# Kernel optimization log

Measured on AMD Instinct MI355X. Metric: run time of the kernel, lower is better.

The kernel has to match this reference:

```python
import jax, jax.numpy as jnp
import numpy as np

D_MODEL = 1024
NUM_HEADS = 16
DK = D_MODEL // NUM_HEADS


def setup_inputs() -> dict:
    key = jax.random.key(0)
    ks = jax.random.split(key, 12)
    B, S, D = 2, 2048, D_MODEL
    s = 1.0 / np.sqrt(D)
    inp = {
        "Q": jax.random.normal(ks[0], (B, S, D), jnp.float32),
        "K": jax.random.normal(ks[1], (B, S, D), jnp.float32),
        "V": jax.random.normal(ks[2], (B, S, D), jnp.float32),
        "Wq": jax.random.uniform(ks[3], (D, D), jnp.float32, -s, s),
        "bq": jax.random.uniform(ks[4], (D,), jnp.float32, -s, s),
        "Wk": jax.random.uniform(ks[5], (D, D), jnp.float32, -s, s),
        "bk": jax.random.uniform(ks[6], (D,), jnp.float32, -s, s),
        "Wv": jax.random.uniform(ks[7], (D, D), jnp.float32, -s, s),
        "bv": jax.random.uniform(ks[8], (D,), jnp.float32, -s, s),
        "Wo": jax.random.uniform(ks[9], (D, D), jnp.float32, -s, s),
        "bo": jax.random.uniform(ks[10], (D,), jnp.float32, -s, s),
    }
    return inp


def reference(Q, K, V, Wq, bq, Wk, bk, Wv, bv, Wo, bo):
    B, S, D = Q.shape
    H, dk = NUM_HEADS, DK
    # projections (torch Linear: x @ W.T + b), split heads -> [B,H,S,dk]
    q = (Q @ Wq.T + bq).reshape(B, S, H, dk).transpose(0, 2, 1, 3)
    k = (K @ Wk.T + bk).reshape(B, S, H, dk).transpose(0, 2, 1, 3)
    v = (V @ Wv.T + bv).reshape(B, S, H, dk).transpose(0, 2, 1, 3)
    scores = jnp.einsum("bhqd,bhkd->bhqk", q, k) / jnp.sqrt(jnp.asarray(dk, q.dtype))
    attn = jax.nn.softmax(scores, axis=-1)
    out = jnp.einsum("bhqk,bhkd->bhqd", attn, v)  # [B,H,S,dk]
    out = out.transpose(0, 2, 1, 3).reshape(B, S, D)
    return out @ Wo.T + bo
```

## Files before the change

### kernel.cpp

```cpp
#include <hip/hip_runtime.h>
#include <stdint.h>


#define AS1 __attribute__((address_space(1)))
#define AS3 __attribute__((address_space(3)))

typedef unsigned short u16;
typedef short s16x8 __attribute__((ext_vector_type(8)));
typedef float f32x4 __attribute__((ext_vector_type(4)));
typedef u16   u16x4 __attribute__((ext_vector_type(4)));

#if defined(__has_builtin)
#if __has_builtin(__builtin_amdgcn_exp2f)
#define EXP2F(x) __builtin_amdgcn_exp2f(x)
#else
#define EXP2F(x) exp2f(x)
#endif
#else
#define EXP2F(x) exp2f(x)
#endif

__device__ __forceinline__ u16 f2b(float f) {
  union { float f; uint32_t u; } v;
  v.f = f;
  uint32_t r = (v.u + 0x7fffu + ((v.u >> 16) & 1u)) >> 16;
  return (u16)r;
}

__device__ __forceinline__ uint32_t cvtpk(float lo, float hi) {
  uint32_t r;
  asm("v_cvt_pk_bf16_f32 %0, %1, %2" : "=v"(r) : "v"(lo), "v"(hi));
  return r;
}

__device__ __forceinline__ f32x4 mfma16(s16x8 a, s16x8 b, f32x4 c) {
  return __builtin_amdgcn_mfma_f32_16x16x32_bf16(a, b, c, 0, 0, 0);
}

__device__ __forceinline__ s16x8 ld_g16(const u16* p) {
  return *reinterpret_cast<const s16x8*>(p);
}

__device__ __forceinline__ void stage16(const u16* g, u16* lds_base) {
  __builtin_amdgcn_global_load_lds((const AS1 unsigned int*)g,
                                   (AS3 unsigned int*)lds_base, 16, 0, 0);
}

struct CvtArgs {
  const float* src[7];
  u16* dst[7];
  int cum[8];
};

__global__ __launch_bounds__(256) void cvt_all(CvtArgs a) {
  const int bx = blockIdx.x;
  int seg = 0;
#pragma unroll
  for (int i = 1; i < 7; ++i) seg += (bx >= a.cum[i]) ? 1 : 0;
  const int off = (bx - a.cum[seg]) * 256 + threadIdx.x;
  float4 f = reinterpret_cast<const float4*>(a.src[seg])[off];
  union { u16 u[4]; uint64_t q; } o;
  o.u[0] = f2b(f.x); o.u[1] = f2b(f.y); o.u[2] = f2b(f.z); o.u[3] = f2b(f.w);
  reinterpret_cast<uint64_t*>(a.dst[seg])[off] = o.q;
}

template <int MODE>
__global__ __launch_bounds__(256) void gemm_bt(const u16* __restrict__ Abase,
                                               const u16* __restrict__ Wbase,
                                               const float* __restrict__ bias0,
                                               const float* __restrict__ bias1,
                                               const float* __restrict__ bias2,
                                               u16* __restrict__ outb,
                                               u16* __restrict__ vtout,
                                               float* __restrict__ outf) {
  __shared__ u16 As[2][128 * 64];
  __shared__ u16 Bs[2][128 * 64];
  const int tid = threadIdx.x;
  const int lane = tid & 63;
  const int w = tid >> 6;
  const int wr = w >> 1, wc = w & 1;

  const int bid = blockIdx.y * 8 + blockIdx.x;
  const int sw = (bid & 7) * 32 + (bid >> 3);
  const int n0 = (sw & 7) * 128;
  const int m0 = (sw >> 3) * 128;
  const int z = (MODE == 0) ? blockIdx.z : 0;
  const float QSC = 0.18033688011112042f;

  const u16* A = Abase + (size_t)z * (4096u * 1024u);
  const u16* W = Wbase + (size_t)z * (1024u * 1024u);
  const float* bias = (MODE == 0) ? (z == 0 ? bias0 : (z == 1 ? bias1 : bias2)) : bias0;
  u16* ob = (MODE == 0) ? (outb + (size_t)z * (4096u * 1024u)) : nullptr;

  const int l15 = lane & 15, l4 = lane >> 4;

  const int sr = lane >> 3;
  const int sx = lane & 7;
  const u16* gA[4];
  const u16* gB[4];
#pragma unroll
  for (int j = 0; j < 4; ++j) {
    const int row = w * 32 + j * 8 + sr;
    const int lc = ((sx ^ (row & 7)) << 3);
    gA[j] = A + (size_t)(m0 + row) * 1024 + lc;
    gB[j] = W + (size_t)(n0 + row) * 1024 + lc;
  }

  f32x4 acc[4][4];
#pragma unroll
  for (int i = 0; i < 4; ++i)
#pragma unroll
    for (int j = 0; j < 4; ++j) acc[i][j] = {0.f, 0.f, 0.f, 0.f};

#pragma unroll
  for (int j = 0; j < 4; ++j) {
    stage16(gA[j], &As[0][(w * 32 + j * 8) * 64]);
    stage16(gB[j], &Bs[0][(w * 32 + j * 8) * 64]);
  }
  __syncthreads();

#pragma unroll 2
  for (int t = 0; t < 16; ++t) {
    const int cur = t & 1;
    if (t + 1 < 16) {
      const int kt = (t + 1) * 64;
#pragma unroll
      for (int j = 0; j < 4; ++j) {
        stage16(gA[j] + kt, &As[cur ^ 1][(w * 32 + j * 8) * 64]);
        stage16(gB[j] + kt, &Bs[cur ^ 1][(w * 32 + j * 8) * 64]);
      }
    }
#pragma unroll
    for (int ks = 0; ks < 2; ++ks) {
      s16x8 af[4], bf[4];
#pragma unroll
      for (int mi = 0; mi < 4; ++mi) {
        const int row = wr * 64 + mi * 16 + l15;
        const int sc_ = (((ks << 2) | l4) ^ (l15 & 7)) << 3;
        af[mi] = *(const s16x8*)&As[cur][row * 64 + sc_];
      }
#pragma unroll
      for (int ni = 0; ni < 4; ++ni) {
        const int row = wc * 64 + ni * 16 + l15;
        const int sc_ = (((ks << 2) | l4) ^ (l15 & 7)) << 3;
        bf[ni] = *(const s16x8*)&Bs[cur][row * 64 + sc_];
      }
      __builtin_amdgcn_s_setprio(1);
#pragma unroll
      for (int mi = 0; mi < 4; ++mi)
#pragma unroll
        for (int ni = 0; ni < 4; ++ni)
          acc[mi][ni] = mfma16(af[mi], bf[ni], acc[mi][ni]);
      __builtin_amdgcn_s_setprio(0);
    }
    __syncthreads();
  }

#pragma unroll
  for (int ni = 0; ni < 4; ++ni) {
    const int col = n0 + wc * 64 + ni * 16 + l15;
    const float bv = bias[col];
#pragma unroll
    for (int mi = 0; mi < 4; ++mi) {
      const int row0 = m0 + wr * 64 + mi * 16 + l4 * 4;
      if (MODE == 0 && z == 2) {
        const int b = row0 >> 11, s0 = row0 & 2047;
        const int pos0 = (s0 & ~31) | ((s0 & 12) << 1) | ((s0 & 16) >> 2);
        const int h = col >> 6, d = col & 63;
        u16x4 pk = {f2b(acc[mi][ni][0] + bv), f2b(acc[mi][ni][1] + bv),
                    f2b(acc[mi][ni][2] + bv), f2b(acc[mi][ni][3] + bv)};
        *(u16x4*)&vtout[((size_t)(b * 16 + h) * 64 + d) * 2048 + pos0] = pk;
      } else {
#pragma unroll
        for (int r = 0; r < 4; ++r) {
          float val = acc[mi][ni][r] + bv;
          const int row = row0 + r;
          if (MODE == 0) {
            if (z == 0) val *= QSC;
            const int b = row >> 11, s = row & 2047;
            const int h = col >> 6, d = col & 63;
            ob[((size_t)(b * 16 + h) * 2048 + s) * 64 + d] = f2b(val);
          } else {
            outf[(size_t)row * 1024 + col] = val;
          }
        }
      }
    }
  }
}

__global__ __launch_bounds__(512, 4) void fattn(const u16* __restrict__ qp,
                                                const u16* __restrict__ kp,
                                                const u16* __restrict__ vt,
                                                u16* __restrict__ ao) {
  __shared__ u16 Kt[2][4096];
  __shared__ u16 Vt[2][4096];

  const int lane = threadIdx.x & 63;
  const int w = threadIdx.x >> 6;
  const int bh = blockIdx.y;
  const int b = bh >> 4, h = bh & 15;
  const int q0 = blockIdx.x * 128 + w * 16;
  const u16* qb = qp + (size_t)bh * (2048 * 64);
  const u16* kb = kp + (size_t)bh * (2048 * 64);
  const u16* vb = vt + (size_t)bh * (64 * 2048);
  const int l15 = lane & 15, l4 = lane >> 4;
  const float THR = 8.0f;

  const int srow = (w << 3) + (lane >> 3);
  const int c0 = (((lane & 7) ^ (srow & 7)) << 3);

  s16x8 qa[2];
#pragma unroll
  for (int ks = 0; ks < 2; ++ks)
    qa[ks] = ld_g16(qb + (size_t)(q0 + l15) * 64 + ks * 32 + l4 * 8);

  s16x8 onesf = {(short)0x3F80, (short)0x3F80, (short)0x3F80, (short)0x3F80,
                 (short)0x3F80, (short)0x3F80, (short)0x3F80, (short)0x3F80};

  f32x4 o[4];
  f32x4 o5 = {0.f, 0.f, 0.f, 0.f};
  float mrun = -1e30f;
#pragma unroll
  for (int ni = 0; ni < 4; ++ni) o[ni] = {0.f, 0.f, 0.f, 0.f};

  stage16(kb + (size_t)srow * 64 + c0, &Kt[0][w * 512]);
  stage16(vb + (size_t)srow * 2048 + c0, &Vt[0][w * 512]);
  __syncthreads();

#pragma unroll 2
  for (int t = 0; t < 32; ++t) {
    const int cur = t & 1;
    if (t + 1 < 32) {
      const int kk = (t + 1) << 6;
      stage16(kb + (size_t)(kk + srow) * 64 + c0, &Kt[cur ^ 1][w * 512]);
      stage16(vb + (size_t)srow * 2048 + kk + c0, &Vt[cur ^ 1][w * 512]);
    }

    f32x4 sc[4];
#pragma unroll
    for (int nk = 0; nk < 4; ++nk) sc[nk] = {0.f, 0.f, 0.f, 0.f};
#pragma unroll
    for (int ks = 0; ks < 2; ++ks) {
      s16x8 kf[4];
#pragma unroll
      for (int nk = 0; nk < 4; ++nk) {
        const int row = nk * 16 + l15;
        const int scx = (((ks << 2) | l4) ^ (l15 & 7)) << 3;
        kf[nk] = *(const s16x8*)&Kt[cur][row * 64 + scx];
      }
      __builtin_amdgcn_s_setprio(1);
#pragma unroll
      for (int nk = 0; nk < 4; ++nk)
        sc[nk] = mfma16(kf[nk], qa[ks], sc[nk]);
      __builtin_amdgcn_s_setprio(0);
    }

    float m01 = fmaxf(fmaxf(sc[0][0], sc[0][1]), fmaxf(sc[0][2], sc[0][3]));
    float m23 = fmaxf(fmaxf(sc[1][0], sc[1][1]), fmaxf(sc[1][2], sc[1][3]));
    float m45 = fmaxf(fmaxf(sc[2][0], sc[2][1]), fmaxf(sc[2][2], sc[2][3]));
    float m67 = fmaxf(fmaxf(sc[3][0], sc[3][1]), fmaxf(sc[3][2], sc[3][3]));
    float m = fmaxf(fmaxf(m01, m23), fmaxf(m45, m67));
    m = fmaxf(m, __shfl_xor(m, 16));
    m = fmaxf(m, __shfl_xor(m, 32));
    const float smax = m;

    if (__any(smax > mrun + THR)) {
      float mn = fmaxf(mrun, smax);
      float alpha = EXP2F(mrun - mn);
      mrun = mn;
#pragma unroll
      for (int r = 0; r < 4; ++r) {
        float ar = __shfl(alpha, l4 * 4 + r);
#pragma unroll
        for (int ni = 0; ni < 4; ++ni) o[ni][r] *= ar;
        o5[r] *= ar;
      }
    }

    float p[4][4];
#pragma unroll
    for (int nk = 0; nk < 4; ++nk)
#pragma unroll
      for (int r = 0; r < 4; ++r)
        p[nk][r] = EXP2F(sc[nk][r] - mrun);

#pragma unroll
    for (int ks = 0; ks < 2; ++ks) {
      union { uint32_t d[4]; s16x8 v; } pa;
      pa.d[0] = cvtpk(p[2 * ks][0], p[2 * ks][1]);
      pa.d[1] = cvtpk(p[2 * ks][2], p[2 * ks][3]);
      pa.d[2] = cvtpk(p[2 * ks + 1][0], p[2 * ks + 1][1]);
      pa.d[3] = cvtpk(p[2 * ks + 1][2], p[2 * ks + 1][3]);
      s16x8 vf[4];
#pragma unroll
      for (int ni = 0; ni < 4; ++ni) {
        const int row = ni * 16 + l15;
        const int scv = (((ks << 2) | l4) ^ (l15 & 7)) << 3;
        vf[ni] = *(const s16x8*)&Vt[cur][row * 64 + scv];
      }
      __builtin_amdgcn_s_setprio(1);
#pragma unroll
      for (int ni = 0; ni < 4; ++ni)
        o[ni] = mfma16(pa.v, vf[ni], o[ni]);
      o5 = mfma16(pa.v, onesf, o5);
      __builtin_amdgcn_s_setprio(0);
    }

    __syncthreads();
  }

#pragma unroll
  for (int r = 0; r < 4; ++r) {
    float inv = 1.0f / o5[r];
    int row = b * 2048 + q0 + l4 * 4 + r;
#pragma unroll
    for (int ni = 0; ni < 4; ++ni)
      ao[(size_t)row * 1024 + h * 64 + ni * 16 + l15] = f2b(o[ni][r] * inv);
  }
}

extern "C" void kernel_launch(void* const* d_in, const int* in_sizes, int n_in,
                              void* d_out, int out_size, void* d_ws, size_t ws_size,
                              hipStream_t stream) {
  const float* Q  = (const float*)d_in[0];
  const float* K  = (const float*)d_in[1];
  const float* V  = (const float*)d_in[2];
  const float* Wq = (const float*)d_in[3];
  const float* bq = (const float*)d_in[4];
  const float* Wk = (const float*)d_in[5];
  const float* bk = (const float*)d_in[6];
  const float* Wv = (const float*)d_in[7];
  const float* bv = (const float*)d_in[8];
  const float* Wo = (const float*)d_in[9];
  const float* bo = (const float*)d_in[10];
  float* out = (float*)d_out;

  const size_t NI = (size_t)4096 * 1024;
  const size_t NW = (size_t)1024 * 1024;
  u16* XB  = (u16*)d_ws;
  u16* WB  = XB + 3 * NI;
  u16* QKV = WB + 4 * NW;
  u16* VT  = QKV + 3 * NI;
  u16* AO  = VT + NI;

  CvtArgs ca;
  ca.src[0] = Q;  ca.dst[0] = XB;
  ca.src[1] = K;  ca.dst[1] = XB + NI;
  ca.src[2] = V;  ca.dst[2] = XB + 2 * NI;
  ca.src[3] = Wq; ca.dst[3] = WB;
  ca.src[4] = Wk; ca.dst[4] = WB + NW;
  ca.src[5] = Wv; ca.dst[5] = WB + 2 * NW;
  ca.src[6] = Wo; ca.dst[6] = WB + 3 * NW;
  ca.cum[0] = 0;     ca.cum[1] = 4096;  ca.cum[2] = 8192;  ca.cum[3] = 12288;
  ca.cum[4] = 13312; ca.cum[5] = 14336; ca.cum[6] = 15360; ca.cum[7] = 16384;
  cvt_all<<<dim3(16384), 256, 0, stream>>>(ca);

  gemm_bt<0><<<dim3(8, 32, 3), 256, 0, stream>>>(XB, WB, bq, bk, bv, QKV, VT, nullptr);
  fattn<<<dim3(16, 32), 512, 0, stream>>>(QKV, QKV + NI, VT, AO);
  gemm_bt<1><<<dim3(8, 32, 1), 256, 0, stream>>>(AO, WB + 3 * NW, bo, nullptr, nullptr,
                                                 nullptr, nullptr, out);
}
```

Baseline: 129.1 us.

## Process two query tiles per wave in flash attention to reuse K/V fragments

Each wave now handles 32 query rows (two 16-row tiles) instead of 16, so every K and V fragment read from LDS feeds twice as many MFMAs, and the grid is halved. The running max is folded into the score accumulator's initial value so the exponent needs no subtraction, and the row max uses v_max3. The cost is higher register pressure (launch bounds relaxed from 4 to 2 blocks per CU) and only 256 blocks, which may leave CUs underfilled on a large GPU.

```diff
diff --git a/kernel.cpp b/kernel.cpp
--- a/kernel.cpp
+++ b/kernel.cpp
@@ -30,6 +30,12 @@
 __device__ __forceinline__ uint32_t cvtpk(float lo, float hi) {
   uint32_t r;
   asm("v_cvt_pk_bf16_f32 %0, %1, %2" : "=v"(r) : "v"(lo), "v"(hi));
+  return r;
+}
+
+__device__ __forceinline__ float max3f(float a, float b, float c) {
+  float r;
+  asm("v_max3_f32 %0, %1, %2, %3" : "=v"(r) : "v"(a), "v"(b), "v"(c));
   return r;
 }
 
@@ -189,7 +195,7 @@
   }
 }
 
-__global__ __launch_bounds__(512, 4) void fattn(const u16* __restrict__ qp,
+__global__ __launch_bounds__(512, 2) void fattn(const u16* __restrict__ qp,
                                                 const u16* __restrict__ kp,
                                                 const u16* __restrict__ vt,
                                                 u16* __restrict__ ao) {
@@ -200,7 +206,7 @@
   const int w = threadIdx.x >> 6;
   const int bh = blockIdx.y;
   const int b = bh >> 4, h = bh & 15;
-  const int q0 = blockIdx.x * 128 + w * 16;
+  const int q0 = blockIdx.x * 256 + w * 32;
   const u16* qb = qp + (size_t)bh * (2048 * 64);
   const u16* kb = kp + (size_t)bh * (2048 * 64);
   const u16* vb = vt + (size_t)bh * (64 * 2048);
@@ -210,19 +216,23 @@
   const int srow = (w << 3) + (lane >> 3);
   const int c0 = (((lane & 7) ^ (srow & 7)) << 3);
 
-  s16x8 qa[2];
-#pragma unroll
-  for (int ks = 0; ks < 2; ++ks)
-    qa[ks] = ld_g16(qb + (size_t)(q0 + l15) * 64 + ks * 32 + l4 * 8);
+  s16x8 qa[2][2];
+#pragma unroll
+  for (int mi = 0; mi < 2; ++mi)
+#pragma unroll
+    for (int ks = 0; ks < 2; ++ks)
+      qa[mi][ks] = ld_g16(qb + (size_t)(q0 + mi * 16 + l15) * 64 + ks * 32 + l4 * 8);
 
   s16x8 onesf = {(short)0x3F80, (short)0x3F80, (short)0x3F80, (short)0x3F80,
                  (short)0x3F80, (short)0x3F80, (short)0x3F80, (short)0x3F80};
 
-  f32x4 o[4];
-  f32x4 o5 = {0.f, 0.f, 0.f, 0.f};
-  float mrun = -1e30f;
-#pragma unroll
-  for (int ni = 0; ni < 4; ++ni) o[ni] = {0.f, 0.f, 0.f, 0.f};
+  f32x4 o[2][4];
+  f32x4 o5[2] = {{0.f, 0.f, 0.f, 0.f}, {0.f, 0.f, 0.f, 0.f}};
+  float mrun[2] = {0.f, 0.f};
+#pragma unroll
+  for (int mi = 0; mi < 2; ++mi)
+#pragma unroll
+    for (int ni = 0; ni < 4; ++ni) o[mi][ni] = {0.f, 0.f, 0.f, 0.f};
 
   stage16(kb + (size_t)srow * 64 + c0, &Kt[0][w * 512]);
   stage16(vb + (size_t)srow * 2048 + c0, &Vt[0][w * 512]);
@@ -237,9 +247,13 @@
       stage16(vb + (size_t)srow * 2048 + kk + c0, &Vt[cur ^ 1][w * 512]);
     }
 
-    f32x4 sc[4];
-#pragma unroll
-    for (int nk = 0; nk < 4; ++nk) sc[nk] = {0.f, 0.f, 0.f, 0.f};
+    f32x4 sc[2][4];
+#pragma unroll
+    for (int mi = 0; mi < 2; ++mi) {
+      const float ini = -mrun[mi];
+#pragma unroll
+      for (int nk = 0; nk < 4; ++nk) sc[mi][nk] = {ini, ini, ini, ini};
+    }
 #pragma unroll
     for (int ks = 0; ks < 2; ++ks) {
       s16x8 kf[4];
@@ -251,73 +265,91 @@
       }
       __builtin_amdgcn_s_setprio(1);
 #pragma unroll
+      for (int mi = 0; mi < 2; ++mi)
+#pragma unroll
+        for (int nk = 0; nk < 4; ++nk)
+          sc[mi][nk] = mfma16(kf[nk], qa[mi][ks], sc[mi][nk]);
+      __builtin_amdgcn_s_setprio(0);
+    }
+
+    float mrel[2];
+#pragma unroll
+    for (int mi = 0; mi < 2; ++mi) {
+      float a = max3f(sc[mi][0][0], sc[mi][0][1], sc[mi][0][2]);
+      float c = max3f(sc[mi][1][0], sc[mi][1][1], sc[mi][1][2]);
+      float d = max3f(sc[mi][2][0], sc[mi][2][1], sc[mi][2][2]);
+      float e = max3f(sc[mi][3][0], sc[mi][3][1], sc[mi][3][2]);
+      float f0 = max3f(sc[mi][0][3], sc[mi][1][3], sc[mi][2][3]);
+      float m = max3f(max3f(a, c, d), max3f(e, f0, sc[mi][3][3]), -1e30f);
+      m = fmaxf(m, __shfl_xor(m, 16));
+      m = fmaxf(m, __shfl_xor(m, 32));
+      mrel[mi] = m;
+    }
+
+    if (__any((mrel[0] > THR) | (mrel[1] > THR))) {
+#pragma unroll
+      for (int mi = 0; mi < 2; ++mi) {
+        const float d = fmaxf(mrel[mi], 0.f);
+        mrun[mi] += d;
+        const float alpha = EXP2F(-d);
+#pragma unroll
+        for (int r = 0; r < 4; ++r) {
+          float ar = __shfl(alpha, l4 * 4 + r);
+#pragma unroll
+          for (int ni = 0; ni < 4; ++ni) o[mi][ni][r] *= ar;
+          o5[mi][r] *= ar;
+        }
+#pragma unroll
+        for (int nk = 0; nk < 4; ++nk)
+#pragma unroll
+          for (int r = 0; r < 4; ++r) sc[mi][nk][r] -= d;
+      }
+    }
+
+#pragma unroll
+    for (int mi = 0; mi < 2; ++mi) {
+      float p[4][4];
+#pragma unroll
       for (int nk = 0; nk < 4; ++nk)
-        sc[nk] = mfma16(kf[nk], qa[ks], sc[nk]);
-      __builtin_amdgcn_s_setprio(0);
-    }
-
-    float m01 = fmaxf(fmaxf(sc[0][0], sc[0][1]), fmaxf(sc[0][2], sc[0][3]));
-    float m23 = fmaxf(fmaxf(sc[1][0], sc[1][1]), fmaxf(sc[1][2], sc[1][3]));
-    float m45 = fmaxf(fmaxf(sc[2][0], sc[2][1]), fmaxf(sc[2][2], sc[2][3]));
-    float m67 = fmaxf(fmaxf(sc[3][0], sc[3][1]), fmaxf(sc[3][2], sc[3][3]));
-    float m = fmaxf(fmaxf(m01, m23), fmaxf(m45, m67));
-    m = fmaxf(m, __shfl_xor(m, 16));
-    m = fmaxf(m, __shfl_xor(m, 32));
-    const float smax = m;
-
-    if (__any(smax > mrun + THR)) {
-      float mn = fmaxf(mrun, smax);
-      float alpha = EXP2F(mrun - mn);
-      mrun = mn;
-#pragma unroll
-      for (int r = 0; r < 4; ++r) {
-        float ar = __shfl(alpha, l4 * 4 + r);
-#pragma unroll
-        for (int ni = 0; ni < 4; ++ni) o[ni][r] *= ar;
-        o5[r] *= ar;
-      }
-    }
-
-    float p[4][4];
-#pragma unroll
-    for (int nk = 0; nk < 4; ++nk)
-#pragma unroll
-      for (int r = 0; r < 4; ++r)
-        p[nk][r] = EXP2F(sc[nk][r] - mrun);
-
-#pragma unroll
-    for (int ks = 0; ks < 2; ++ks) {
-      union { uint32_t d[4]; s16x8 v; } pa;
-      pa.d[0] = cvtpk(p[2 * ks][0], p[2 * ks][1]);
-      pa.d[1] = cvtpk(p[2 * ks][2], p[2 * ks][3]);
-      pa.d[2] = cvtpk(p[2 * ks + 1][0], p[2 * ks + 1][1]);
-      pa.d[3] = cvtpk(p[2 * ks + 1][2], p[2 * ks + 1][3]);
-      s16x8 vf[4];
-#pragma unroll
-      for (int ni = 0; ni < 4; ++ni) {
-        const int row = ni * 16 + l15;
-        const int scv = (((ks << 2) | l4) ^ (l15 & 7)) << 3;
-        vf[ni] = *(const s16x8*)&Vt[cur][row * 64 + scv];
-      }
-      __builtin_amdgcn_s_setprio(1);
+#pragma unroll
+        for (int r = 0; r < 4; ++r)
+          p[nk][r] = EXP2F(sc[mi][nk][r]);
+#pragma unroll
+      for (int ks = 0; ks < 2; ++ks) {
+        union { uint32_t d[4]; s16x8 v; } pa;
+        pa.d[0] = cvtpk(p[2 * ks][0], p[2 * ks][1]);
+        pa.d[1] = cvtpk(p[2 * ks][2], p[2 * ks][3]);
+        pa.d[2] = cvtpk(p[2 * ks + 1][0], p[2 * ks + 1][1]);
+        pa.d[3] = cvtpk(p[2 * ks + 1][2], p[2 * ks + 1][3]);
+        s16x8 vf[4];
+#pragma unroll
+        for (int ni = 0; ni < 4; ++ni) {
+          const int row = ni * 16 + l15;
+          const int scv = (((ks << 2) | l4) ^ (l15 & 7)) << 3;
+          vf[ni] = *(const s16x8*)&Vt[cur][row * 64 + scv];
+        }
+        __builtin_amdgcn_s_setprio(1);
+#pragma unroll
+        for (int ni = 0; ni < 4; ++ni)
+          o[mi][ni] = mfma16(pa.v, vf[ni], o[mi][ni]);
+        o5[mi] = mfma16(pa.v, onesf, o5[mi]);
+        __builtin_amdgcn_s_setprio(0);
+      }
+    }
+
+    __syncthreads();
+  }
+
+#pragma unroll
+  for (int mi = 0; mi < 2; ++mi)
+#pragma unroll
+    for (int r = 0; r < 4; ++r) {
+      float inv = 1.0f / o5[mi][r];
+      int row = b * 2048 + q0 + mi * 16 + l4 * 4 + r;
 #pragma unroll
       for (int ni = 0; ni < 4; ++ni)
-        o[ni] = mfma16(pa.v, vf[ni], o[ni]);
-      o5 = mfma16(pa.v, onesf, o5);
-      __builtin_amdgcn_s_setprio(0);
-    }
-
-    __syncthreads();
-  }
-
-#pragma unroll
-  for (int r = 0; r < 4; ++r) {
-    float inv = 1.0f / o5[r];
-    int row = b * 2048 + q0 + l4 * 4 + r;
-#pragma unroll
-    for (int ni = 0; ni < 4; ++ni)
-      ao[(size_t)row * 1024 + h * 64 + ni * 16 + l15] = f2b(o[ni][r] * inv);
-  }
+        ao[(size_t)row * 1024 + h * 64 + ni * 16 + l15] = f2b(o[mi][ni][r] * inv);
+    }
 }
 
 extern "C" void kernel_launch(void* const* d_in, const int* in_sizes, int n_in,
@@ -357,7 +389,7 @@
   cvt_all<<<dim3(16384), 256, 0, stream>>>(ca);
 
   gemm_bt<0><<<dim3(8, 32, 3), 256, 0, stream>>>(XB, WB, bq, bk, bv, QKV, VT, nullptr);
-  fattn<<<dim3(16, 32), 512, 0, stream>>>(QKV, QKV + NI, VT, AO);
+  fattn<<<dim3(8, 32), 512, 0, stream>>>(QKV, QKV + NI, VT, AO);
   gemm_bt<1><<<dim3(8, 32, 1), 256, 0, stream>>>(AO, WB + 3 * NW, bo, nullptr, nullptr,
                                                  nullptr, nullptr, out);
 }
```

Result: no change. 127.3 us (-1.4%).

## Switch flash attention to 32x32x16 MFMA with 32 query rows per wave

Applied to the files above, without the earlier changes.

Rewrites the attention inner loop to use 32x32x16 bf16 MFMAs, with each wave owning 32 query rows. The grid is halved and launch bounds are relaxed to match. The running max is folded into the score accumulator's initial value, and the row sum is accumulated with VALU adds instead of an extra MFMA against a ones vector. V^T's permuted layout in the projection GEMM is changed to match the new MFMA operand order. This cuts MFMA instruction count and LDS fragment reloads per tile, at the cost of higher register pressure, lower occupancy and fewer blocks (256) in flight.

```diff
diff --git a/kernel.cpp b/kernel.cpp
--- a/kernel.cpp
+++ b/kernel.cpp
@@ -8,6 +8,7 @@
 typedef unsigned short u16;
 typedef short s16x8 __attribute__((ext_vector_type(8)));
 typedef float f32x4 __attribute__((ext_vector_type(4)));
+typedef float f32x16 __attribute__((ext_vector_type(16)));
 typedef u16   u16x4 __attribute__((ext_vector_type(4)));
 
 #if defined(__has_builtin)
@@ -33,8 +34,18 @@
   return r;
 }
 
+__device__ __forceinline__ float max3f(float a, float b, float c) {
+  float r;
+  asm("v_max3_f32 %0, %1, %2, %3" : "=v"(r) : "v"(a), "v"(b), "v"(c));
+  return r;
+}
+
 __device__ __forceinline__ f32x4 mfma16(s16x8 a, s16x8 b, f32x4 c) {
   return __builtin_amdgcn_mfma_f32_16x16x32_bf16(a, b, c, 0, 0, 0);
+}
+
+__device__ __forceinline__ f32x16 mfma32(s16x8 a, s16x8 b, f32x16 c) {
+  return __builtin_amdgcn_mfma_f32_32x32x16_bf16(a, b, c, 0, 0, 0);
 }
 
 __device__ __forceinline__ s16x8 ld_g16(const u16* p) {
@@ -165,7 +176,7 @@
       const int row0 = m0 + wr * 64 + mi * 16 + l4 * 4;
       if (MODE == 0 && z == 2) {
         const int b = row0 >> 11, s0 = row0 & 2047;
-        const int pos0 = (s0 & ~31) | ((s0 & 12) << 1) | ((s0 & 16) >> 2);
+        const int pos0 = (s0 & ~15) | ((s0 & 4) << 1) | ((s0 & 8) >> 1);
         const int h = col >> 6, d = col & 63;
         u16x4 pk = {f2b(acc[mi][ni][0] + bv), f2b(acc[mi][ni][1] + bv),
                     f2b(acc[mi][ni][2] + bv), f2b(acc[mi][ni][3] + bv)};
@@ -189,7 +200,7 @@
   }
 }
 
-__global__ __launch_bounds__(512, 4) void fattn(const u16* __restrict__ qp,
+__global__ __launch_bounds__(512, 2) void fattn(const u16* __restrict__ qp,
                                                 const u16* __restrict__ kp,
                                                 const u16* __restrict__ vt,
                                                 u16* __restrict__ ao) {
@@ -200,29 +211,27 @@
   const int w = threadIdx.x >> 6;
   const int bh = blockIdx.y;
   const int b = bh >> 4, h = bh & 15;
-  const int q0 = blockIdx.x * 128 + w * 16;
+  const int q0 = blockIdx.x * 256 + w * 32;
   const u16* qb = qp + (size_t)bh * (2048 * 64);
   const u16* kb = kp + (size_t)bh * (2048 * 64);
   const u16* vb = vt + (size_t)bh * (64 * 2048);
-  const int l15 = lane & 15, l4 = lane >> 4;
+  const int l31 = lane & 31, hl = lane >> 5;
+  const int x7 = l31 & 7;
   const float THR = 8.0f;
 
   const int srow = (w << 3) + (lane >> 3);
   const int c0 = (((lane & 7) ^ (srow & 7)) << 3);
 
-  s16x8 qa[2];
-#pragma unroll
-  for (int ks = 0; ks < 2; ++ks)
-    qa[ks] = ld_g16(qb + (size_t)(q0 + l15) * 64 + ks * 32 + l4 * 8);
-
-  s16x8 onesf = {(short)0x3F80, (short)0x3F80, (short)0x3F80, (short)0x3F80,
-                 (short)0x3F80, (short)0x3F80, (short)0x3F80, (short)0x3F80};
-
-  f32x4 o[4];
-  f32x4 o5 = {0.f, 0.f, 0.f, 0.f};
-  float mrun = -1e30f;
-#pragma unroll
-  for (int ni = 0; ni < 4; ++ni) o[ni] = {0.f, 0.f, 0.f, 0.f};
+  s16x8 qa[4];
+#pragma unroll
+  for (int kc = 0; kc < 4; ++kc)
+    qa[kc] = ld_g16(qb + (size_t)(q0 + l31) * 64 + kc * 16 + hl * 8);
+
+  f32x16 o[2];
+  float lsum = 0.f;
+  float mrun = 0.f;
+#pragma unroll
+  for (int r = 0; r < 16; ++r) { o[0][r] = 0.f; o[1][r] = 0.f; }
 
   stage16(kb + (size_t)srow * 64 + c0, &Kt[0][w * 512]);
   stage16(vb + (size_t)srow * 2048 + c0, &Vt[0][w * 512]);
@@ -237,86 +246,83 @@
       stage16(vb + (size_t)srow * 2048 + kk + c0, &Vt[cur ^ 1][w * 512]);
     }
 
-    f32x4 sc[4];
-#pragma unroll
-    for (int nk = 0; nk < 4; ++nk) sc[nk] = {0.f, 0.f, 0.f, 0.f};
-#pragma unroll
-    for (int ks = 0; ks < 2; ++ks) {
+    f32x16 sc[2];
+#pragma unroll
+    for (int r = 0; r < 16; ++r) { sc[0][r] = -mrun; sc[1][r] = -mrun; }
+#pragma unroll
+    for (int nk = 0; nk < 2; ++nk) {
       s16x8 kf[4];
 #pragma unroll
-      for (int nk = 0; nk < 4; ++nk) {
-        const int row = nk * 16 + l15;
-        const int scx = (((ks << 2) | l4) ^ (l15 & 7)) << 3;
-        kf[nk] = *(const s16x8*)&Kt[cur][row * 64 + scx];
-      }
+      for (int kc = 0; kc < 4; ++kc)
+        kf[kc] = *(const s16x8*)&Kt[cur][(nk * 32 + l31) * 64 +
+                                         ((((kc << 1) | hl) ^ x7) << 3)];
       __builtin_amdgcn_s_setprio(1);
 #pragma unroll
-      for (int nk = 0; nk < 4; ++nk)
-        sc[nk] = mfma16(kf[nk], qa[ks], sc[nk]);
+      for (int kc = 0; kc < 4; ++kc)
+        sc[nk] = mfma32(kf[kc], qa[kc], sc[nk]);
       __builtin_amdgcn_s_setprio(0);
     }
 
-    float m01 = fmaxf(fmaxf(sc[0][0], sc[0][1]), fmaxf(sc[0][2], sc[0][3]));
-    float m23 = fmaxf(fmaxf(sc[1][0], sc[1][1]), fmaxf(sc[1][2], sc[1][3]));
-    float m45 = fmaxf(fmaxf(sc[2][0], sc[2][1]), fmaxf(sc[2][2], sc[2][3]));
-    float m67 = fmaxf(fmaxf(sc[3][0], sc[3][1]), fmaxf(sc[3][2], sc[3][3]));
-    float m = fmaxf(fmaxf(m01, m23), fmaxf(m45, m67));
-    m = fmaxf(m, __shfl_xor(m, 16));
+    float m = -1e30f;
+#pragma unroll
+    for (int nk = 0; nk < 2; ++nk)
+#pragma unroll
+      for (int r = 0; r < 16; r += 2)
+        m = max3f(m, sc[nk][r], sc[nk][r + 1]);
     m = fmaxf(m, __shfl_xor(m, 32));
-    const float smax = m;
-
-    if (__any(smax > mrun + THR)) {
-      float mn = fmaxf(mrun, smax);
-      float alpha = EXP2F(mrun - mn);
-      mrun = mn;
-#pragma unroll
-      for (int r = 0; r < 4; ++r) {
-        float ar = __shfl(alpha, l4 * 4 + r);
-#pragma unroll
-        for (int ni = 0; ni < 4; ++ni) o[ni][r] *= ar;
-        o5[r] *= ar;
-      }
-    }
-
-    float p[4][4];
-#pragma unroll
-    for (int nk = 0; nk < 4; ++nk)
-#pragma unroll
-      for (int r = 0; r < 4; ++r)
-        p[nk][r] = EXP2F(sc[nk][r] - mrun);
-
-#pragma unroll
-    for (int ks = 0; ks < 2; ++ks) {
-      union { uint32_t d[4]; s16x8 v; } pa;
-      pa.d[0] = cvtpk(p[2 * ks][0], p[2 * ks][1]);
-      pa.d[1] = cvtpk(p[2 * ks][2], p[2 * ks][3]);
-      pa.d[2] = cvtpk(p[2 * ks + 1][0], p[2 * ks + 1][1]);
-      pa.d[3] = cvtpk(p[2 * ks + 1][2], p[2 * ks + 1][3]);
-      s16x8 vf[4];
-#pragma unroll
-      for (int ni = 0; ni < 4; ++ni) {
-        const int row = ni * 16 + l15;
-        const int scv = (((ks << 2) | l4) ^ (l15 & 7)) << 3;
-        vf[ni] = *(const s16x8*)&Vt[cur][row * 64 + scv];
-      }
-      __builtin_amdgcn_s_setprio(1);
-#pragma unroll
-      for (int ni = 0; ni < 4; ++ni)
-        o[ni] = mfma16(pa.v, vf[ni], o[ni]);
-      o5 = mfma16(pa.v, onesf, o5);
-      __builtin_amdgcn_s_setprio(0);
+
+    if (__any(m > THR)) {
+      const float d = fmaxf(m, 0.f);
+      mrun += d;
+      const float alpha = EXP2F(-d);
+      lsum *= alpha;
+#pragma unroll
+      for (int r = 0; r < 16; ++r) { sc[0][r] -= d; sc[1][r] -= d; }
+#pragma unroll
+      for (int r = 0; r < 16; ++r) {
+        float ar = __shfl(alpha, (r & 3) + 8 * (r >> 2) + 4 * hl);
+        o[0][r] *= ar; o[1][r] *= ar;
+      }
+    }
+
+#pragma unroll
+    for (int nk = 0; nk < 2; ++nk) {
+      float p[16];
+#pragma unroll
+      for (int r = 0; r < 16; ++r) p[r] = EXP2F(sc[nk][r]);
+#pragma unroll
+      for (int r = 0; r < 16; ++r) lsum += p[r];
+#pragma unroll
+      for (int kc = 0; kc < 2; ++kc) {
+        union { uint32_t d[4]; s16x8 v; } pa;
+        pa.d[0] = cvtpk(p[kc * 8 + 0], p[kc * 8 + 1]);
+        pa.d[1] = cvtpk(p[kc * 8 + 2], p[kc * 8 + 3]);
+        pa.d[2] = cvtpk(p[kc * 8 + 4], p[kc * 8 + 5]);
+        pa.d[3] = cvtpk(p[kc * 8 + 6], p[kc * 8 + 7]);
+        const int chunk = nk * 4 + kc * 2 + hl;
+#pragma unroll
+        for (int dt = 0; dt < 2; ++dt) {
+          s16x8 vf = *(const s16x8*)&Vt[cur][(dt * 32 + l31) * 64 +
+                                             ((chunk ^ x7) << 3)];
+          __builtin_amdgcn_s_setprio(1);
+          o[dt] = mfma32(pa.v, vf, o[dt]);
+          __builtin_amdgcn_s_setprio(0);
+        }
+      }
     }
 
     __syncthreads();
   }
 
-#pragma unroll
-  for (int r = 0; r < 4; ++r) {
-    float inv = 1.0f / o5[r];
-    int row = b * 2048 + q0 + l4 * 4 + r;
-#pragma unroll
-    for (int ni = 0; ni < 4; ++ni)
-      ao[(size_t)row * 1024 + h * 64 + ni * 16 + l15] = f2b(o[ni][r] * inv);
+  lsum += __shfl_xor(lsum, 32);
+#pragma unroll
+  for (int r = 0; r < 16; ++r) {
+    const int qreg = (r & 3) + 8 * (r >> 2) + 4 * hl;
+    const float inv = 1.0f / __shfl(lsum, qreg);
+    const int row = b * 2048 + q0 + qreg;
+#pragma unroll
+    for (int dt = 0; dt < 2; ++dt)
+      ao[(size_t)row * 1024 + h * 64 + dt * 32 + l31] = f2b(o[dt][r] * inv);
   }
 }
 
@@ -357,7 +363,7 @@
   cvt_all<<<dim3(16384), 256, 0, stream>>>(ca);
 
   gemm_bt<0><<<dim3(8, 32, 3), 256, 0, stream>>>(XB, WB, bq, bk, bv, QKV, VT, nullptr);
-  fattn<<<dim3(16, 32), 512, 0, stream>>>(QKV, QKV + NI, VT, AO);
+  fattn<<<dim3(8, 32), 512, 0, stream>>>(QKV, QKV + NI, VT, AO);
   gemm_bt<1><<<dim3(8, 32, 1), 256, 0, stream>>>(AO, WB + 3 * NW, bo, nullptr, nullptr,
                                                  nullptr, nullptr, out);
 }
```

Result: no change. 128.0 us (-0.9%).
